# Kernel optimization log

Hardware: AMD Instinct MI355X
Metric: run time of the kernel (lower is better)

## Reference

```python
import jax, jax.numpy as jnp
import numpy as np

B, CIN, G, H, HW, WMIX = 128, 64, 8, 14, 16, 16  # batch, in-ch, groups, spatial, mixed width


def setup_inputs() -> dict:
    key = jax.random.key(0)
    k1, k2, k3 = jax.random.split(key, 3)
    x = jax.random.normal(k1, (B, CIN, G, H, H), dtype=jnp.float32)
    w_conv = jax.random.normal(k2, (G, 3, 3, 32), dtype=jnp.float32)   # weights[0]
    w_mix = jax.random.normal(k3, (CIN, WMIX), dtype=jnp.float32)       # weights[1]
    return {"x": x, "w_conv": w_conv, "w_mix": w_mix}


def _unfold3(t, axis, size):
    # torch F.unfold with kernel (3,1), padding (1,0) along `axis`: zero-pad by 1
    # and stack the 3 shifted windows as a new axis inserted at `axis`.
    pad = [(0, 0)] * t.ndim
    pad[axis] = (1, 1)
    p = jnp.pad(t, pad)
    slices = []
    for k in range(3):
        idx = [slice(None)] * t.ndim
        idx[axis] = slice(k, k + size)
        slices.append(p[tuple(idx)])
    return jnp.stack(slices, axis=axis)


def reference(x, w_conv, w_mix):
    # channel mix: (B, 64, 8, 14, 14) x (64, 16) -> (B, 8, 14, 14, 16)
    t4 = jnp.einsum('kjmnl,ji->kmnli', x, w_mix)
    # first unfold along H (axis 3): (B, 8, 14, 3, 14, 16)
    u1 = _unfold3(t4, 3, H)
    # second unfold along H (now axis 4): (B, 8, 14, 3, 3, 14, 16)
    u2 = _unfold3(u1, 4, H)
    # permute (0,1,2,5,4,3,6) -> (B, 8, 14, 14, 3, 3, 16)
    t5 = jnp.transpose(u2, (0, 1, 2, 5, 4, 3, 6))
    # conv channel mix: contract group(8) and both 3-taps -> (B, 14, 14, 16, 32)
    t6 = jnp.einsum('mlonikp,likj->monpj', t5, w_conv)
    # (B, 14, 14, 32, 16) -> (B, 14, 14, 512)
    t7 = jnp.transpose(t6, (0, 1, 2, 4, 3)).reshape(B, H, H, 512)
    t7 = jnp.roll(t7, 1, axis=1)  # shift_direction fixed to +1
    return jnp.transpose(t7, (0, 3, 1, 2))  # (B, 512, 14, 14)
```

## Files before the change

kernel.cpp:

```cpp
#include <hip/hip_runtime.h>

static constexpr int NB   = 128;
static constexpr int NCIN = 64;
static constexpr int NG   = 8;
static constexpr int NH   = 14;
static constexpr int NP   = 16;
static constexpr int NJ   = 32;
static constexpr int HH   = NH * NH;
static constexpr int LROW = 20;

__global__ __launch_bounds__(64) void mix_kernel(const float* __restrict__ x,
                                                 const float* __restrict__ wmix,
                                                 float* __restrict__ t4) {
    int t     = blockIdx.x * 64 + threadIdx.x;
    int squad = t % 49;
    int bg    = t / 49;
    int b     = bg >> 3;
    int g     = bg & 7;

    float acc[4][NP];
#pragma unroll
    for (int q = 0; q < 4; q++)
#pragma unroll
        for (int p = 0; p < NP; p++) acc[q][p] = 0.f;

    const float* xbase = x + (size_t)b * (NCIN * NG * HH) + (size_t)g * HH + squad * 4;

#pragma unroll 4
    for (int j = 0; j < NCIN; j++) {
        float4 xv = *reinterpret_cast<const float4*>(xbase + (size_t)j * (NG * HH));
#pragma unroll
        for (int p = 0; p < NP; p++) {
            float w = wmix[j * NP + p];
            acc[0][p] += xv.x * w;
            acc[1][p] += xv.y * w;
            acc[2][p] += xv.z * w;
            acc[3][p] += xv.w * w;
        }
    }

    float* tb = t4 + ((size_t)bg * HH + squad * 4) * NP;
#pragma unroll
    for (int q = 0; q < 4; q++)
#pragma unroll
        for (int p4 = 0; p4 < 4; p4++) {
            *reinterpret_cast<float4*>(tb + q * NP + p4 * 4) =
                make_float4(acc[q][p4 * 4 + 0], acc[q][p4 * 4 + 1],
                            acc[q][p4 * 4 + 2], acc[q][p4 * 4 + 3]);
        }
}

__global__ __launch_bounds__(128) void conv_kernel(const float* __restrict__ t4,
                                                   const float* __restrict__ wconv,
                                                   float* __restrict__ out) {
    __shared__ __align__(16) float lds[512 * 15];
    float* t4s = lds;
    float* w2s = lds + 2560;
    float* wcs = lds + 3840;

    const int tid   = threadIdx.x;
    const int b     = blockIdx.x / NH;
    const int o     = blockIdx.x % NH;
    const int o_src = (o + NH - 1) % NH;

    const float* tsl = t4 + ((size_t)b * NG * HH + (size_t)o_src * NH) * NP;
#pragma unroll
    for (int r = 0; r < 14; r++) {
        int idx = r * 128 + tid;
        int g   = idx / 224;
        int rem = idx % 224;
        int l   = rem / 16;
        int p   = rem % 16;
        t4s[(g * 16 + p) * LROW + (l + 2)] = tsl[(size_t)g * HH * NP + l * 16 + p];
    }
#pragma unroll
    for (int r = 0; r < 6; r++) {
        int idx = r * 128 + tid;
        int gp  = idx / 6;
        int s   = idx % 6;
        int l2  = (s < 2) ? s : (14 + s);
        t4s[gp * LROW + l2] = 0.f;
    }
#pragma unroll
    for (int r = 0; r < 10; r++) {
        int idx = r * 128 + tid;
        int g   = idx / 160;
        int di  = (idx / 32) % 5;
        int j   = idx % 32;
        int ilo = di > 2 ? di - 2 : 0;
        int ihi = di < 2 ? di : 2;
        float s = 0.f;
        for (int i = ilo; i <= ihi; i++) {
            int k = di - i;
            s += wconv[((g * 3 + i) * 3 + k) * 32 + j];
        }
        w2s[idx] = s;
    }
#pragma unroll
    for (int r = 0; r < 4; r++) {
        int idx = r * 128 + tid;
        int sel = idx / 256;
        int g   = (idx / 32) % 8;
        int j   = idx % 32;
        wcs[idx] = wconv[(g * 9 + (sel ? 6 : 2)) * 32 + j];
    }
    __syncthreads();

    const int p     = tid & 15;
    const int jg    = tid >> 4;
    const int jbase = jg * 4;

    float acc[NH][4];
#pragma unroll
    for (int n = 0; n < NH; n++) {
        acc[n][0] = 0.f; acc[n][1] = 0.f; acc[n][2] = 0.f; acc[n][3] = 0.f;
    }

    for (int g = 0; g < NG; g++) {
        float row[LROW];
        const float* rp = &t4s[(g * 16 + p) * LROW];
#pragma unroll
        for (int q = 0; q < 5; q++) {
            float4 v = *reinterpret_cast<const float4*>(rp + q * 4);
            row[q * 4 + 0] = v.x; row[q * 4 + 1] = v.y;
            row[q * 4 + 2] = v.z; row[q * 4 + 3] = v.w;
        }
#pragma unroll
        for (int di = 0; di < 5; di++) {
            float4 w = *reinterpret_cast<const float4*>(&w2s[(g * 5 + di) * 32 + jbase]);
#pragma unroll
            for (int n = 0; n < NH; n++) {
                float rv = row[n + di];
                acc[n][0] += rv * w.x;
                acc[n][1] += rv * w.y;
                acc[n][2] += rv * w.z;
                acc[n][3] += rv * w.w;
            }
        }
        float4 c0 = *reinterpret_cast<const float4*>(&wcs[g * 32 + jbase]);
        float4 c1 = *reinterpret_cast<const float4*>(&wcs[256 + g * 32 + jbase]);
        float r2 = row[2], r15 = row[15];
        acc[0][0]  -= r2  * c0.x; acc[0][1]  -= r2  * c0.y;
        acc[0][2]  -= r2  * c0.z; acc[0][3]  -= r2  * c0.w;
        acc[13][0] -= r15 * c1.x; acc[13][1] -= r15 * c1.y;
        acc[13][2] -= r15 * c1.z; acc[13][3] -= r15 * c1.w;
    }

    __syncthreads();

#pragma unroll
    for (int jj = 0; jj < 4; jj++) {
        int c = (jbase + jj) * 16 + p;
#pragma unroll
        for (int n = 0; n < NH; n++) lds[c * 15 + n] = acc[n][jj];
    }
    __syncthreads();

    float* ob = out + (size_t)b * 512 * HH + (size_t)o * NH;
#pragma unroll
    for (int r = 0; r < 56; r++) {
        int idx = r * 128 + tid;
        int c   = idx / 14;
        int n   = idx % 14;
        ob[(size_t)c * HH + n] = lds[c * 15 + n];
    }
}

extern "C" void kernel_launch(void* const* d_in, const int* in_sizes, int n_in,
                              void* d_out, int out_size, void* d_ws, size_t ws_size,
                              hipStream_t stream) {
    const float* x     = (const float*)d_in[0];
    const float* wconv = (const float*)d_in[1];
    const float* wmix  = (const float*)d_in[2];
    float* out = (float*)d_out;
    float* t4  = (float*)d_ws;

    mix_kernel<<<784, 64, 0, stream>>>(x, wmix, t4);
    conv_kernel<<<NB * NH, 128, 0, stream>>>(t4, wconv, out);
}
```

Baseline: 160.3 us.

## Use 256-thread blocks, smaller per-thread tiles, and halved LDS output staging

The mix kernel now gives each thread one spatial position instead of four, running in 256-thread blocks. The conv kernel doubles its block to 256 threads, with each thread holding two output channels instead of four. It also stages the output through LDS in two halves so shared memory drops from about 30KB to about 17KB. The t4 tile is loaded with float4 reads. The aim is higher occupancy and lower register pressure, at the cost of less register reuse of weights and inputs and extra barriers.

```diff
diff --git a/kernel.cpp b/kernel.cpp
--- a/kernel.cpp
+++ b/kernel.cpp
@@ -9,51 +9,41 @@
 static constexpr int HH   = NH * NH;
 static constexpr int LROW = 20;
 
-__global__ __launch_bounds__(64) void mix_kernel(const float* __restrict__ x,
-                                                 const float* __restrict__ wmix,
-                                                 float* __restrict__ t4) {
-    int t     = blockIdx.x * 64 + threadIdx.x;
-    int squad = t % 49;
-    int bg    = t / 49;
-    int b     = bg >> 3;
-    int g     = bg & 7;
+__global__ __launch_bounds__(256) void mix_kernel(const float* __restrict__ x,
+                                                  const float* __restrict__ wmix,
+                                                  float* __restrict__ t4) {
+    int gid = blockIdx.x * 256 + threadIdx.x;
+    int ml  = gid % HH;
+    int bg  = gid / HH;
+    int b   = bg >> 3;
+    int g   = bg & 7;
 
-    float acc[4][NP];
+    float acc[NP];
 #pragma unroll
-    for (int q = 0; q < 4; q++)
-#pragma unroll
-        for (int p = 0; p < NP; p++) acc[q][p] = 0.f;
+    for (int p = 0; p < NP; p++) acc[p] = 0.f;
 
-    const float* xbase = x + (size_t)b * (NCIN * NG * HH) + (size_t)g * HH + squad * 4;
+    const float* xb = x + (size_t)b * (NCIN * NG * HH) + (size_t)g * HH + ml;
 
 #pragma unroll 4
     for (int j = 0; j < NCIN; j++) {
-        float4 xv = *reinterpret_cast<const float4*>(xbase + (size_t)j * (NG * HH));
+        float xv = xb[(size_t)j * (NG * HH)];
 #pragma unroll
-        for (int p = 0; p < NP; p++) {
-            float w = wmix[j * NP + p];
-            acc[0][p] += xv.x * w;
-            acc[1][p] += xv.y * w;
-            acc[2][p] += xv.z * w;
-            acc[3][p] += xv.w * w;
-        }
+        for (int p = 0; p < NP; p++) acc[p] += xv * wmix[j * NP + p];
     }
 
-    float* tb = t4 + ((size_t)bg * HH + squad * 4) * NP;
+    float* tb = t4 + (size_t)gid * NP;
 #pragma unroll
-    for (int q = 0; q < 4; q++)
-#pragma unroll
-        for (int p4 = 0; p4 < 4; p4++) {
-            *reinterpret_cast<float4*>(tb + q * NP + p4 * 4) =
-                make_float4(acc[q][p4 * 4 + 0], acc[q][p4 * 4 + 1],
-                            acc[q][p4 * 4 + 2], acc[q][p4 * 4 + 3]);
-        }
+    for (int p4 = 0; p4 < 4; p4++) {
+        *reinterpret_cast<float4*>(tb + p4 * 4) =
+            make_float4(acc[p4 * 4 + 0], acc[p4 * 4 + 1],
+                        acc[p4 * 4 + 2], acc[p4 * 4 + 3]);
+    }
 }
 
-__global__ __launch_bounds__(128) void conv_kernel(const float* __restrict__ t4,
+__global__ __launch_bounds__(256) void conv_kernel(const float* __restrict__ t4,
                                                    const float* __restrict__ wconv,
                                                    float* __restrict__ out) {
-    __shared__ __align__(16) float lds[512 * 15];
+    __shared__ __align__(16) float lds[4352];
     float* t4s = lds;
     float* w2s = lds + 2560;
     float* wcs = lds + 3840;
@@ -63,27 +53,34 @@
     const int o     = blockIdx.x % NH;
     const int o_src = (o + NH - 1) % NH;
 
-    const float* tsl = t4 + ((size_t)b * NG * HH + (size_t)o_src * NH) * NP;
+    const float4* tsl4 = reinterpret_cast<const float4*>(
+        t4 + ((size_t)b * NG * HH + (size_t)o_src * NH) * NP);
 #pragma unroll
-    for (int r = 0; r < 14; r++) {
-        int idx = r * 128 + tid;
-        int g   = idx / 224;
-        int rem = idx % 224;
-        int l   = rem / 16;
-        int p   = rem % 16;
-        t4s[(g * 16 + p) * LROW + (l + 2)] = tsl[(size_t)g * HH * NP + l * 16 + p];
+    for (int r = 0; r < 2; r++) {
+        int idx = r * 256 + tid;
+        if (idx < 448) {
+            int g  = idx / 56;
+            int rr = idx % 56;
+            int l  = rr >> 2;
+            int p0 = (rr & 3) * 4;
+            float4 v = tsl4[(size_t)g * (HH * NP / 4) + rr];
+            t4s[(g * 16 + p0 + 0) * LROW + (l + 2)] = v.x;
+            t4s[(g * 16 + p0 + 1) * LROW + (l + 2)] = v.y;
+            t4s[(g * 16 + p0 + 2) * LROW + (l + 2)] = v.z;
+            t4s[(g * 16 + p0 + 3) * LROW + (l + 2)] = v.w;
+        }
     }
 #pragma unroll
-    for (int r = 0; r < 6; r++) {
-        int idx = r * 128 + tid;
+    for (int r = 0; r < 3; r++) {
+        int idx = r * 256 + tid;
         int gp  = idx / 6;
         int s   = idx % 6;
         int l2  = (s < 2) ? s : (14 + s);
         t4s[gp * LROW + l2] = 0.f;
     }
 #pragma unroll
-    for (int r = 0; r < 10; r++) {
-        int idx = r * 128 + tid;
+    for (int r = 0; r < 5; r++) {
+        int idx = r * 256 + tid;
         int g   = idx / 160;
         int di  = (idx / 32) % 5;
         int j   = idx % 32;
@@ -97,8 +94,8 @@
         w2s[idx] = s;
     }
 #pragma unroll
-    for (int r = 0; r < 4; r++) {
-        int idx = r * 128 + tid;
+    for (int r = 0; r < 2; r++) {
+        int idx = r * 256 + tid;
         int sel = idx / 256;
         int g   = (idx / 32) % 8;
         int j   = idx % 32;
@@ -106,15 +103,13 @@
     }
     __syncthreads();
 
-    const int p     = tid & 15;
-    const int jg    = tid >> 4;
-    const int jbase = jg * 4;
+    const int p  = tid & 15;
+    const int jh = tid >> 4;
+    const int jb = jh * 2;
 
-    float acc[NH][4];
+    float acc[NH][2];
 #pragma unroll
-    for (int n = 0; n < NH; n++) {
-        acc[n][0] = 0.f; acc[n][1] = 0.f; acc[n][2] = 0.f; acc[n][3] = 0.f;
-    }
+    for (int n = 0; n < NH; n++) { acc[n][0] = 0.f; acc[n][1] = 0.f; }
 
     for (int g = 0; g < NG; g++) {
         float row[LROW];
@@ -127,42 +122,44 @@
         }
 #pragma unroll
         for (int di = 0; di < 5; di++) {
-            float4 w = *reinterpret_cast<const float4*>(&w2s[(g * 5 + di) * 32 + jbase]);
+            float2 w = *reinterpret_cast<const float2*>(&w2s[(g * 5 + di) * 32 + jb]);
 #pragma unroll
             for (int n = 0; n < NH; n++) {
                 float rv = row[n + di];
                 acc[n][0] += rv * w.x;
                 acc[n][1] += rv * w.y;
-                acc[n][2] += rv * w.z;
-                acc[n][3] += rv * w.w;
             }
         }
-        float4 c0 = *reinterpret_cast<const float4*>(&wcs[g * 32 + jbase]);
-        float4 c1 = *reinterpret_cast<const float4*>(&wcs[256 + g * 32 + jbase]);
+        float2 c0 = *reinterpret_cast<const float2*>(&wcs[g * 32 + jb]);
+        float2 c1 = *reinterpret_cast<const float2*>(&wcs[256 + g * 32 + jb]);
         float r2 = row[2], r15 = row[15];
         acc[0][0]  -= r2  * c0.x; acc[0][1]  -= r2  * c0.y;
-        acc[0][2]  -= r2  * c0.z; acc[0][3]  -= r2  * c0.w;
         acc[13][0] -= r15 * c1.x; acc[13][1] -= r15 * c1.y;
-        acc[13][2] -= r15 * c1.z; acc[13][3] -= r15 * c1.w;
     }
 
     __syncthreads();
 
+    float* obase = out + (size_t)b * 512 * HH + (size_t)o * NH;
 #pragma unroll
-    for (int jj = 0; jj < 4; jj++) {
-        int c = (jbase + jj) * 16 + p;
+    for (int h = 0; h < 2; h++) {
+        if ((jh >> 3) == h) {
 #pragma unroll
-        for (int n = 0; n < NH; n++) lds[c * 15 + n] = acc[n][jj];
-    }
-    __syncthreads();
-
-    float* ob = out + (size_t)b * 512 * HH + (size_t)o * NH;
+            for (int jj = 0; jj < 2; jj++) {
+                int cl = (jb + jj) * 16 + p - h * 256;
 #pragma unroll
-    for (int r = 0; r < 56; r++) {
-        int idx = r * 128 + tid;
-        int c   = idx / 14;
-        int n   = idx % 14;
-        ob[(size_t)c * HH + n] = lds[c * 15 + n];
+                for (int n = 0; n < NH; n++) lds[cl * 15 + n] = acc[n][jj];
+            }
+        }
+        __syncthreads();
+        float* ob = obase + (size_t)(h * 256) * HH;
+#pragma unroll
+        for (int r = 0; r < 14; r++) {
+            int idx = r * 256 + tid;
+            int c   = idx / 14;
+            int n   = idx % 14;
+            ob[(size_t)c * HH + n] = lds[c * 15 + n];
+        }
+        __syncthreads();
     }
 }
 
@@ -175,6 +172,6 @@
     float* out = (float*)d_out;
     float* t4  = (float*)d_ws;
 
-    mix_kernel<<<784, 64, 0, stream>>>(x, wmix, t4);
-    conv_kernel<<<NB * NH, 128, 0, stream>>>(t4, wconv, out);
+    mix_kernel<<<784, 256, 0, stream>>>(x, wmix, t4);
+    conv_kernel<<<NB * NH, 256, 0, stream>>>(t4, wconv, out);
 }
```

After: 138.1 us. -13.8%, faster.
